# Kernel optimization log

Measured on AMD Instinct MI355X. Metric: run time of the kernel, lower is better.

The kernel has to match this reference:

```python
import jax, jax.numpy as jnp
import numpy as np

N = 50000      # nodes
E = 250000     # edges (pairs) per key
DIN = 256
DOUT = 256
OH = 16        # one_hot_length
T = 2          # params['t']


def setup_inputs() -> dict:
    key = jax.random.key(0)
    ks = jax.random.split(key, 16)
    s_in = 1.0 / np.float32(np.sqrt(DIN))
    s_tr = 1.0 / np.float32(np.sqrt(DIN + OH))
    return {
        "h": jax.random.normal(ks[0], (N, DIN), jnp.float32),
        "pairs_k0": jax.random.randint(ks[1], (T, E), 0, N),
        "pairs_k1": jax.random.randint(ks[2], (T, E), 0, N),
        "degrees_k0": jax.random.uniform(ks[3], (T, E, OH), jnp.float32),
        "degrees_k1": jax.random.uniform(ks[4], (T, E, OH), jnp.float32),
        "scatter_k0": jax.random.randint(ks[5], (E,), 0, N),
        "scatter_k1": jax.random.randint(ks[6], (E,), 0, N),
        "W_lin": jax.random.normal(ks[7], (DIN, DOUT), jnp.float32) * s_in,
        "b_lin": jax.random.normal(ks[8], (DOUT,), jnp.float32) * 0.01,
        "W_k0": jax.random.normal(ks[9], (DIN + OH, DOUT), jnp.float32) * s_tr,
        "b_k0": jax.random.normal(ks[10], (DOUT,), jnp.float32) * 0.01,
        "W_k1": jax.random.normal(ks[11], (DIN + OH, DOUT), jnp.float32) * s_tr,
        "b_k1": jax.random.normal(ks[12], (DOUT,), jnp.float32) * 0.01,
        "eps_k0": jnp.zeros((1,), jnp.float32),
        "eps_k1": jnp.zeros((1,), jnp.float32),
    }


def _key_term(h, pairs, degrees, W, b, scatter, eps):
    # combination == 'multi': product over t of sigmoid(Linear([h[pairs_i], deg_i]))
    h_temp = jnp.ones((pairs.shape[1], W.shape[1]), h.dtype)
    for i in range(T):
        h_t = jnp.concatenate([h[pairs[i]], degrees[i]], axis=1)  # [E, DIN+OH]
        h_temp = h_temp * jax.nn.sigmoid(h_t @ W + b)             # [E, DOUT]
    h_sum = jax.ops.segment_sum(h_temp, scatter, num_segments=N)  # [N, DOUT]
    return (1.0 + eps) * h_sum                                    # scalar eps (shape [1])


def reference(h, pairs_k0, pairs_k1, degrees_k0, degrees_k1,
              scatter_k0, scatter_k1, W_lin, b_lin,
              W_k0, b_k0, W_k1, b_k1, eps_k0, eps_k1):
    h3 = h @ W_lin + b_lin
    h3 = h3 + _key_term(h, pairs_k0, degrees_k0, W_k0, b_k0, scatter_k0, eps_k0)
    h3 = h3 + _key_term(h, pairs_k1, degrees_k1, W_k1, b_k1, scatter_k1, eps_k1)
    return h3
```

## Files before the change

### kernel.cpp

```cpp
#include <hip/hip_runtime.h>
#include <hip/hip_bf16.h>

#define N_NODES 50000
#define N_EDGES 250000
#define DIN_ 256
#define DOUT_ 256
#define OH_ 16
#define KF_ 288
#define NBLK_EDGE ((N_EDGES + 63) / 64)
#define SCAN_TOT (2 * N_NODES)
#define SCAN_NB ((SCAN_TOT + 255) / 256)

typedef short short8 __attribute__((ext_vector_type(8)));
typedef float f32x4 __attribute__((ext_vector_type(4)));

__device__ __forceinline__ unsigned short f2bf(float f) {
    unsigned u = __builtin_bit_cast(unsigned, f);
    return (unsigned short)((u + 0x7fffu + ((u >> 16) & 1u)) >> 16);
}

__device__ __forceinline__ uint4 pack8(float f0, float f1, float f2, float f3,
                                       float f4, float f5, float f6, float f7) {
    uint4 u;
    u.x = (unsigned)f2bf(f0) | ((unsigned)f2bf(f1) << 16);
    u.y = (unsigned)f2bf(f2) | ((unsigned)f2bf(f3) << 16);
    u.z = (unsigned)f2bf(f4) | ((unsigned)f2bf(f5) << 16);
    u.w = (unsigned)f2bf(f6) | ((unsigned)f2bf(f7) << 16);
    return u;
}

__device__ __forceinline__ float fast_rcp(float x) {
#if __has_builtin(__builtin_amdgcn_rcpf)
    return __builtin_amdgcn_rcpf(x);
#else
    return 1.0f / x;
#endif
}

__device__ __forceinline__ void gl_lds16(const void* g, void* l) {
    __builtin_amdgcn_global_load_lds(
        (const __attribute__((address_space(1))) unsigned int*)g,
        (__attribute__((address_space(3))) unsigned int*)l, 16, 0, 0);
}

__global__ void hist_kernel(const int* __restrict__ sc0, const int* __restrict__ sc1,
                            int* __restrict__ hist) {
    int e = blockIdx.x * 256 + threadIdx.x;
    if (e < N_EDGES) {
        atomicAdd(&hist[sc0[e]], 1);
        atomicAdd(&hist[N_NODES + sc1[e]], 1);
    }
}

__global__ void scan_pass1(const int* __restrict__ hist, int* __restrict__ partials) {
    __shared__ int sdata[256];
    int gid = blockIdx.x * 256 + threadIdx.x;
    sdata[threadIdx.x] = (gid < SCAN_TOT) ? hist[gid] : 0;
    __syncthreads();
    for (int d = 128; d > 0; d >>= 1) {
        if (threadIdx.x < d) sdata[threadIdx.x] += sdata[threadIdx.x + d];
        __syncthreads();
    }
    if (threadIdx.x == 0) partials[blockIdx.x] = sdata[0];
}

__global__ __launch_bounds__(512) void scan_pass2(int* __restrict__ partials) {
    __shared__ int s[512];
    int t = threadIdx.x;
    s[t] = (t < SCAN_NB) ? partials[t] : 0;
    __syncthreads();
    for (int d = 1; d < 512; d <<= 1) {
        int add = (t >= d) ? s[t - d] : 0;
        __syncthreads();
        s[t] += add;
        __syncthreads();
    }
    if (t < SCAN_NB) partials[t] = (t == 0) ? 0 : s[t - 1];
}

__global__ void scan_pass3(const int* __restrict__ hist, const int* __restrict__ partials,
                           int* __restrict__ offs) {
    __shared__ int s[256];
    int gid = blockIdx.x * 256 + threadIdx.x;
    int t = threadIdx.x;
    int v = (gid < SCAN_TOT) ? hist[gid] : 0;
    s[t] = v;
    __syncthreads();
    for (int d = 1; d < 256; d <<= 1) {
        int add = (t >= d) ? s[t - d] : 0;
        __syncthreads();
        s[t] += add;
        __syncthreads();
    }
    if (gid < SCAN_TOT) offs[gid] = partials[blockIdx.x] + s[t] - v;
}

__global__ void rank_kernel(const int* __restrict__ sc0, const int* __restrict__ sc1,
                            int* __restrict__ offs, int* __restrict__ order,
                            int* __restrict__ keys) {
    int e = blockIdx.x * 256 + threadIdx.x;
    if (e < N_EDGES) {
        int k0 = sc0[e];
        int p = atomicAdd(&offs[k0], 1);
        order[p] = e; keys[p] = k0;
        int k1 = sc1[e];
        int q = atomicAdd(&offs[N_NODES + k1], 1);
        order[q] = e; keys[q] = k1;
    }
}

__global__ void prep_weights(const float* __restrict__ W_lin,
                             const float* __restrict__ W_k0,
                             const float* __restrict__ W_k1,
                             unsigned short* __restrict__ WT_lin,
                             unsigned short* __restrict__ WT_k0,
                             unsigned short* __restrict__ WT_k1) {
    int idx = blockIdx.x * 256 + threadIdx.x;
    if (idx < DOUT_ * DIN_) {
        int n = idx >> 8, k = idx & 255;
        WT_lin[idx] = f2bf(W_lin[k * DOUT_ + n]);
    }
    if (idx < DOUT_ * KF_) {
        int n = idx / KF_, k = idx - n * KF_;
        float v0 = 0.f, v1 = 0.f;
        if (k < DIN_ + OH_) {
            v0 = W_k0[k * DOUT_ + n];
            v1 = W_k1[k * DOUT_ + n];
        }
        WT_k0[idx] = f2bf(v0);
        WT_k1[idx] = f2bf(v1);
    }
}

__global__ void conv_h(const float* __restrict__ h, unsigned short* __restrict__ hbf) {
    int idx = blockIdx.x * 256 + threadIdx.x;
    const float4* s = (const float4*)(h + (size_t)idx * 8);
    float4 a = s[0], b = s[1];
    ((uint4*)hbf)[idx] = pack8(a.x, a.y, a.z, a.w, b.x, b.y, b.z, b.w);
}

__global__ __launch_bounds__(256) void main_gemm(const unsigned short* __restrict__ hbf,
                                                 const unsigned short* __restrict__ WT,
                                                 const float* __restrict__ bias,
                                                 float* __restrict__ out) {
    __shared__ unsigned short Alds[2][64][32];
    __shared__ unsigned short Blds[2][256][32];
    __shared__ float bias_lds[256];
    int tid = threadIdx.x;
    int w = tid >> 6, ln = tid & 63, l15 = ln & 15;
    int row0 = blockIdx.x * 64;
    bias_lds[tid] = bias[tid];

    int ar = row0 + w * 16 + (ln >> 2);
    if (ar >= N_NODES) ar = N_NODES - 1;
    int qs = (ln & 3) ^ ((ln >> 3) & 3);
    const unsigned short* asrc = hbf + (size_t)ar * DIN_ + qs * 8;
    int brow = w * 64;
    int swz = ((ln >> 4) ^ ((l15 >> 1) & 3)) * 8;

    f32x4 acc[16];
#pragma unroll
    for (int j = 0; j < 16; ++j) acc[j] = (f32x4)(0.f);

    gl_lds16(asrc, &Alds[0][w * 16][0]);
#pragma unroll
    for (int i = 0; i < 4; ++i) {
        int n = brow + i * 16 + (ln >> 2);
        gl_lds16(WT + (size_t)n * DIN_ + qs * 8, &Blds[0][brow + i * 16][0]);
    }
    __syncthreads();

    int buf = 0;
    for (int kk = 0; kk < 8; ++kk) {
        if (kk < 7) {
            gl_lds16(asrc + (kk + 1) * 32, &Alds[buf ^ 1][w * 16][0]);
#pragma unroll
            for (int i = 0; i < 4; ++i) {
                int n = brow + i * 16 + (ln >> 2);
                gl_lds16(WT + (size_t)n * DIN_ + (kk + 1) * 32 + qs * 8,
                         &Blds[buf ^ 1][brow + i * 16][0]);
            }
        }
        short8 af = *(const short8*)&Alds[buf][w * 16 + l15][swz];
#pragma unroll
        for (int j = 0; j < 16; ++j) {
            short8 bf = *(const short8*)&Blds[buf][j * 16 + l15][swz];
            acc[j] = __builtin_amdgcn_mfma_f32_16x16x32_bf16(af, bf, acc[j], 0, 0, 0);
        }
        __syncthreads();
        buf ^= 1;
    }

    int rbase = row0 + w * 16 + ((ln >> 4) << 2);
#pragma unroll
    for (int j = 0; j < 16; ++j) {
        int n = j * 16 + l15;
        float bv = bias_lds[n];
#pragma unroll
        for (int i = 0; i < 4; ++i) {
            int rr = rbase + i;
            if (rr < N_NODES) out[(size_t)rr * DOUT_ + n] = acc[j][i] + bv;
        }
    }
}

__global__ __launch_bounds__(256) void edge_gemm(const unsigned short* __restrict__ hbf,
                                                 const int* __restrict__ pairs0,
                                                 const int* __restrict__ pairs1,
                                                 const float* __restrict__ deg0,
                                                 const float* __restrict__ deg1,
                                                 const int* __restrict__ order_all,
                                                 const int* __restrict__ keys_all,
                                                 const unsigned short* __restrict__ WT0,
                                                 const unsigned short* __restrict__ WT1,
                                                 const float* __restrict__ bias0,
                                                 const float* __restrict__ bias1,
                                                 const float* __restrict__ eps0,
                                                 const float* __restrict__ eps1,
                                                 float* __restrict__ out) {
    __shared__ unsigned short Alds[2][2][64][32];
    __shared__ unsigned short Blds[2][256][32];
    __shared__ float bias_lds[256];
    __shared__ int tgt[64];
    int kb = (blockIdx.x >= NBLK_EDGE) ? 1 : 0;
    int bx = blockIdx.x - kb * NBLK_EDGE;
    const int* pairs = kb ? pairs1 : pairs0;
    const float* degrees = kb ? deg1 : deg0;
    const int* order_k = order_all + kb * N_EDGES;
    const int* keys_k  = keys_all + kb * N_EDGES;
    const unsigned short* WT = kb ? WT1 : WT0;
    const float* bias = kb ? bias1 : bias0;
    const float* eps  = kb ? eps1 : eps0;

    int tid = threadIdx.x;
    int w = tid >> 6, ln = tid & 63, l15 = ln & 15;
    int e0 = bx * 64;
    bias_lds[tid] = bias[tid];
    if (tid < 64) {
        int s = e0 + tid;
        tgt[tid] = (s < N_EDGES) ? keys_k[s] : -1;
    }

    int sA = e0 + w * 16 + (ln >> 2);
    if (sA >= N_EDGES) sA = N_EDGES - 1;
    int eA = order_k[sA];
    int p0 = pairs[eA];
    int p1 = pairs[N_EDGES + eA];
    int qs = (ln & 3) ^ ((ln >> 3) & 3);
    const unsigned short* a0src = hbf + (size_t)p0 * DIN_ + qs * 8;
    const unsigned short* a1src = hbf + (size_t)p1 * DIN_ + qs * 8;
    int brow = w * 64;
    int swz = ((ln >> 4) ^ ((l15 >> 1) & 3)) * 8;

    int r8 = tid >> 2, q8 = tid & 3;
    int m8 = (q8 ^ ((r8 >> 1) & 3)) * 8;
    int s8 = e0 + r8;
    if (s8 >= N_EDGES) s8 = N_EDGES - 1;
    int e8 = order_k[s8];

    f32x4 acc0[16], acc1[16];
#pragma unroll
    for (int j = 0; j < 16; ++j) { acc0[j] = (f32x4)(0.f); acc1[j] = (f32x4)(0.f); }

    gl_lds16(a0src, &Alds[0][0][w * 16][0]);
    gl_lds16(a1src, &Alds[0][1][w * 16][0]);
#pragma unroll
    for (int i = 0; i < 4; ++i) {
        int n = brow + i * 16 + (ln >> 2);
        gl_lds16(WT + (size_t)n * KF_ + qs * 8, &Blds[0][brow + i * 16][0]);
    }
    __syncthreads();

    int buf = 0;
    for (int kk = 0; kk < 9; ++kk) {
        if (kk < 8) {
#pragma unroll
            for (int i = 0; i < 4; ++i) {
                int n = brow + i * 16 + (ln >> 2);
                gl_lds16(WT + (size_t)n * KF_ + (kk + 1) * 32 + qs * 8,
                         &Blds[buf ^ 1][brow + i * 16][0]);
            }
            if (kk < 7) {
                gl_lds16(a0src + (kk + 1) * 32, &Alds[buf ^ 1][0][w * 16][0]);
                gl_lds16(a1src + (kk + 1) * 32, &Alds[buf ^ 1][1][w * 16][0]);
            } else {
#pragma unroll
                for (int t = 0; t < 2; ++t) {
                    uint4 v = make_uint4(0u, 0u, 0u, 0u);
                    if (q8 < 2) {
                        const float4* s4 = (const float4*)(degrees +
                            ((size_t)t * N_EDGES + e8) * OH_ + q8 * 8);
                        float4 a = s4[0], b = s4[1];
                        v = pack8(a.x, a.y, a.z, a.w, b.x, b.y, b.z, b.w);
                    }
                    *(uint4*)&Alds[buf ^ 1][t][r8][m8] = v;
                }
            }
        }
        short8 a0f = *(const short8*)&Alds[buf][0][w * 16 + l15][swz];
        short8 a1f = *(const short8*)&Alds[buf][1][w * 16 + l15][swz];
#pragma unroll
        for (int j = 0; j < 16; ++j) {
            short8 bf = *(const short8*)&Blds[buf][j * 16 + l15][swz];
            acc0[j] = __builtin_amdgcn_mfma_f32_16x16x32_bf16(a0f, bf, acc0[j], 0, 0, 0);
            acc1[j] = __builtin_amdgcn_mfma_f32_16x16x32_bf16(a1f, bf, acc1[j], 0, 0, 0);
        }
        __syncthreads();
        buf ^= 1;
    }

    float* red = (float*)&Blds[0][0][0];
    float epv = 1.0f + eps[0];
    int rloc = w * 16 + ((ln >> 4) << 2);
    int c = tid & 63, Rb = (tid >> 6) * 16;

#pragma unroll
    for (int jc = 0; jc < 4; ++jc) {
#pragma unroll
        for (int jj = 0; jj < 4; ++jj) {
            float bv = bias_lds[(jc * 4 + jj) * 16 + l15];
#pragma unroll
            for (int i = 0; i < 4; ++i) {
                int row = rloc + i;
                float v = 0.f;
                if (e0 + row < N_EDGES) {
                    float a = acc0[jc * 4 + jj][i] + bv;
                    float b = acc1[jc * 4 + jj][i] + bv;
                    float ea = __expf(-a), eb = __expf(-b);
                    v = epv * fast_rcp((1.f + ea) * (1.f + eb));
                }
                red[row * 68 + jj * 16 + l15] = v;
            }
        }
        __syncthreads();
        int n = jc * 64 + c;
        int runkey = tgt[Rb];
        float runsum = red[Rb * 68 + c];
        for (int r = Rb + 1; r < Rb + 16; ++r) {
            int k = tgt[r];
            float val = red[r * 68 + c];
            if (k != runkey) {
                if (runkey >= 0) atomicAdd(&out[(size_t)runkey * DOUT_ + n], runsum);
                runkey = k;
                runsum = val;
            } else {
                runsum += val;
            }
        }
        if (runkey >= 0) atomicAdd(&out[(size_t)runkey * DOUT_ + n], runsum);
        __syncthreads();
    }
}

extern "C" void kernel_launch(void* const* d_in, const int* in_sizes, int n_in,
                              void* d_out, int out_size, void* d_ws, size_t ws_size,
                              hipStream_t stream) {
    const float* h        = (const float*)d_in[0];
    const int*   pairs_k0 = (const int*)d_in[1];
    const int*   pairs_k1 = (const int*)d_in[2];
    const float* deg_k0   = (const float*)d_in[3];
    const float* deg_k1   = (const float*)d_in[4];
    const int*   sc_k0    = (const int*)d_in[5];
    const int*   sc_k1    = (const int*)d_in[6];
    const float* W_lin    = (const float*)d_in[7];
    const float* b_lin    = (const float*)d_in[8];
    const float* W_k0     = (const float*)d_in[9];
    const float* b_k0     = (const float*)d_in[10];
    const float* W_k1     = (const float*)d_in[11];
    const float* b_k1     = (const float*)d_in[12];
    const float* eps_k0   = (const float*)d_in[13];
    const float* eps_k1   = (const float*)d_in[14];
    float* out = (float*)d_out;

    size_t ush_elems = (size_t)DOUT_ * DIN_ + 2 * (size_t)DOUT_ * KF_ + (size_t)N_NODES * DIN_;
    size_t int_elems = 2 * (size_t)N_NODES * 2 + 2 * (size_t)N_EDGES * 2 + 512;
    size_t need = ush_elems * sizeof(unsigned short) + int_elems * sizeof(int);
    if (ws_size < need) return;

    unsigned short* WT_lin = (unsigned short*)d_ws;
    unsigned short* WT_k0  = WT_lin + DOUT_ * DIN_;
    unsigned short* WT_k1  = WT_k0 + DOUT_ * KF_;
    unsigned short* h_bf   = WT_k1 + DOUT_ * KF_;
    int* hist     = (int*)(h_bf + (size_t)N_NODES * DIN_);
    int* offs     = hist + 2 * N_NODES;
    int* order    = offs + 2 * N_NODES;
    int* keys     = order + 2 * N_EDGES;
    int* partials = keys + 2 * N_EDGES;

    hipMemsetAsync(hist, 0, 2 * N_NODES * sizeof(int), stream);
    hist_kernel<<<(N_EDGES + 255) / 256, 256, 0, stream>>>(sc_k0, sc_k1, hist);
    scan_pass1<<<SCAN_NB, 256, 0, stream>>>(hist, partials);
    scan_pass2<<<1, 512, 0, stream>>>(partials);
    scan_pass3<<<SCAN_NB, 256, 0, stream>>>(hist, partials, offs);
    rank_kernel<<<(N_EDGES + 255) / 256, 256, 0, stream>>>(sc_k0, sc_k1, offs, order, keys);

    prep_weights<<<(DOUT_ * KF_ + 255) / 256, 256, 0, stream>>>(W_lin, W_k0, W_k1,
                                                                WT_lin, WT_k0, WT_k1);
    conv_h<<<(N_NODES * DIN_ / 8) / 256, 256, 0, stream>>>(h, h_bf);
    main_gemm<<<(N_NODES + 63) / 64, 256, 0, stream>>>(h_bf, WT_lin, b_lin, out);
    edge_gemm<<<2 * NBLK_EDGE, 256, 0, stream>>>(h_bf, pairs_k0, pairs_k1, deg_k0, deg_k1,
                                                 order, keys, WT_k0, WT_k1, b_k0, b_k1,
                                                 eps_k0, eps_k1, out);
}
```

Baseline: 426.2 us.

## Precompute per-node h@W projections and gather them in the edge kernel

Because h[pairs]@W[:256] equals (h@W[:256])[pairs], a new per-node GEMM computes G = h@W + b for each key once over the 50000 nodes and stores it in bf16. The edge kernel then only does the small 16-wide degree GEMM per edge and gathers G rows for both pair endpoints before the sigmoid product and segmented atomic reduction. This removes the 250000x256x256 per-edge GEMM in exchange for a node GEMM, extra workspace, bf16 rounding of G, and scattered 2-byte gathers from G.

Result: no change. 427.1 us (+0.2%).

```diff
diff --git a/kernel.cpp b/kernel.cpp
--- a/kernel.cpp
+++ b/kernel.cpp
@@ -8,6 +8,7 @@
 #define OH_ 16
 #define KF_ 288
 #define NBLK_EDGE ((N_EDGES + 63) / 64)
+#define NBLK_G ((N_NODES + 63) / 64)
 #define SCAN_TOT (2 * N_NODES)
 #define SCAN_NB ((SCAN_TOT + 255) / 256)
 
@@ -17,6 +18,10 @@
 __device__ __forceinline__ unsigned short f2bf(float f) {
     unsigned u = __builtin_bit_cast(unsigned, f);
     return (unsigned short)((u + 0x7fffu + ((u >> 16) & 1u)) >> 16);
+}
+
+__device__ __forceinline__ float bf2f(unsigned short v) {
+    return __builtin_bit_cast(float, (unsigned)v << 16);
 }
 
 __device__ __forceinline__ uint4 pack8(float f0, float f1, float f2, float f3,
@@ -204,151 +209,189 @@
     }
 }
 
-__global__ __launch_bounds__(256) void edge_gemm(const unsigned short* __restrict__ hbf,
-                                                 const int* __restrict__ pairs0,
-                                                 const int* __restrict__ pairs1,
-                                                 const float* __restrict__ deg0,
-                                                 const float* __restrict__ deg1,
-                                                 const int* __restrict__ order_all,
-                                                 const int* __restrict__ keys_all,
-                                                 const unsigned short* __restrict__ WT0,
-                                                 const unsigned short* __restrict__ WT1,
-                                                 const float* __restrict__ bias0,
-                                                 const float* __restrict__ bias1,
-                                                 const float* __restrict__ eps0,
-                                                 const float* __restrict__ eps1,
-                                                 float* __restrict__ out) {
-    __shared__ unsigned short Alds[2][2][64][32];
+__global__ __launch_bounds__(256) void g_gemm(const unsigned short* __restrict__ hbf,
+                                              const unsigned short* __restrict__ WT0,
+                                              const unsigned short* __restrict__ WT1,
+                                              const float* __restrict__ b0,
+                                              const float* __restrict__ b1,
+                                              unsigned short* __restrict__ G0,
+                                              unsigned short* __restrict__ G1) {
+    __shared__ unsigned short Alds[2][64][32];
     __shared__ unsigned short Blds[2][256][32];
     __shared__ float bias_lds[256];
-    __shared__ int tgt[64];
+    int kb = (blockIdx.x >= NBLK_G) ? 1 : 0;
+    int bx = blockIdx.x - kb * NBLK_G;
+    const unsigned short* WT = kb ? WT1 : WT0;
+    const float* bias = kb ? b1 : b0;
+    unsigned short* G = kb ? G1 : G0;
+
+    int tid = threadIdx.x;
+    int w = tid >> 6, ln = tid & 63, l15 = ln & 15;
+    int row0 = bx * 64;
+    bias_lds[tid] = bias[tid];
+
+    int ar = row0 + w * 16 + (ln >> 2);
+    if (ar >= N_NODES) ar = N_NODES - 1;
+    int qs = (ln & 3) ^ ((ln >> 3) & 3);
+    const unsigned short* asrc = hbf + (size_t)ar * DIN_ + qs * 8;
+    int brow = w * 64;
+    int swz = ((ln >> 4) ^ ((l15 >> 1) & 3)) * 8;
+
+    f32x4 acc[16];
+#pragma unroll
+    for (int j = 0; j < 16; ++j) acc[j] = (f32x4)(0.f);
+
+    gl_lds16(asrc, &Alds[0][w * 16][0]);
+#pragma unroll
+    for (int i = 0; i < 4; ++i) {
+        int n = brow + i * 16 + (ln >> 2);
+        gl_lds16(WT + (size_t)n * KF_ + qs * 8, &Blds[0][brow + i * 16][0]);
+    }
+    __syncthreads();
+
+    int buf = 0;
+    for (int kk = 0; kk < 8; ++kk) {
+        if (kk < 7) {
+            gl_lds16(asrc + (kk + 1) * 32, &Alds[buf ^ 1][w * 16][0]);
+#pragma unroll
+            for (int i = 0; i < 4; ++i) {
+                int n = brow + i * 16 + (ln >> 2);
+                gl_lds16(WT + (size_t)n * KF_ + (kk + 1) * 32 + qs * 8,
+                         &Blds[buf ^ 1][brow + i * 16][0]);
+            }
+        }
+        short8 af = *(const short8*)&Alds[buf][w * 16 + l15][swz];
+#pragma unroll
+        for (int j = 0; j < 16; ++j) {
+            short8 bf = *(const short8*)&Blds[buf][j * 16 + l15][swz];
+            acc[j] = __builtin_amdgcn_mfma_f32_16x16x32_bf16(af, bf, acc[j], 0, 0, 0);
+        }
+        __syncthreads();
+        buf ^= 1;
+    }
+
+    int rbase = row0 + w * 16 + ((ln >> 4) << 2);
+#pragma unroll
+    for (int j = 0; j < 16; ++j) {
+        int n = j * 16 + l15;
+        float bv = bias_lds[n];
+#pragma unroll
+        for (int i = 0; i < 4; ++i) {
+            int rr = rbase + i;
+            if (rr < N_NODES) G[(size_t)rr * DOUT_ + n] = f2bf(acc[j][i] + bv);
+        }
+    }
+}
+
+__global__ __launch_bounds__(256) void edge_fused(const unsigned short* __restrict__ Gk0,
+                                                  const unsigned short* __restrict__ Gk1,
+                                                  const int* __restrict__ pairs0,
+                                                  const int* __restrict__ pairs1,
+                                                  const float* __restrict__ deg0,
+                                                  const float* __restrict__ deg1,
+                                                  const int* __restrict__ order_all,
+                                                  const int* __restrict__ keys_all,
+                                                  const unsigned short* __restrict__ WT0,
+                                                  const unsigned short* __restrict__ WT1,
+                                                  const float* __restrict__ eps0,
+                                                  const float* __restrict__ eps1,
+                                                  float* __restrict__ out) {
+    __shared__ float red0[64][68];
+    __shared__ float red1[64][68];
+    __shared__ int tgt[64], pl0[64], pl1[64], el[64];
     int kb = (blockIdx.x >= NBLK_EDGE) ? 1 : 0;
     int bx = blockIdx.x - kb * NBLK_EDGE;
+    const unsigned short* G = kb ? Gk1 : Gk0;
     const int* pairs = kb ? pairs1 : pairs0;
     const float* degrees = kb ? deg1 : deg0;
     const int* order_k = order_all + kb * N_EDGES;
     const int* keys_k  = keys_all + kb * N_EDGES;
     const unsigned short* WT = kb ? WT1 : WT0;
-    const float* bias = kb ? bias1 : bias0;
-    const float* eps  = kb ? eps1 : eps0;
+    float epv = 1.0f + (kb ? eps1[0] : eps0[0]);
 
     int tid = threadIdx.x;
-    int w = tid >> 6, ln = tid & 63, l15 = ln & 15;
+    int w = tid >> 6, ln = tid & 63, l15 = ln & 15, ks = ln >> 4;
     int e0 = bx * 64;
-    bias_lds[tid] = bias[tid];
     if (tid < 64) {
         int s = e0 + tid;
+        int sc = (s < N_EDGES) ? s : N_EDGES - 1;
+        int e = order_k[sc];
+        el[tid]  = e;
         tgt[tid] = (s < N_EDGES) ? keys_k[s] : -1;
-    }
-
-    int sA = e0 + w * 16 + (ln >> 2);
-    if (sA >= N_EDGES) sA = N_EDGES - 1;
-    int eA = order_k[sA];
-    int p0 = pairs[eA];
-    int p1 = pairs[N_EDGES + eA];
-    int qs = (ln & 3) ^ ((ln >> 3) & 3);
-    const unsigned short* a0src = hbf + (size_t)p0 * DIN_ + qs * 8;
-    const unsigned short* a1src = hbf + (size_t)p1 * DIN_ + qs * 8;
-    int brow = w * 64;
-    int swz = ((ln >> 4) ^ ((l15 >> 1) & 3)) * 8;
-
-    int r8 = tid >> 2, q8 = tid & 3;
-    int m8 = (q8 ^ ((r8 >> 1) & 3)) * 8;
-    int s8 = e0 + r8;
-    if (s8 >= N_EDGES) s8 = N_EDGES - 1;
-    int e8 = order_k[s8];
-
-    f32x4 acc0[16], acc1[16];
-#pragma unroll
-    for (int j = 0; j < 16; ++j) { acc0[j] = (f32x4)(0.f); acc1[j] = (f32x4)(0.f); }
-
-    gl_lds16(a0src, &Alds[0][0][w * 16][0]);
-    gl_lds16(a1src, &Alds[0][1][w * 16][0]);
-#pragma unroll
-    for (int i = 0; i < 4; ++i) {
-        int n = brow + i * 16 + (ln >> 2);
-        gl_lds16(WT + (size_t)n * KF_ + qs * 8, &Blds[0][brow + i * 16][0]);
-    }
-    __syncthreads();
-
-    int buf = 0;
-    for (int kk = 0; kk < 9; ++kk) {
-        if (kk < 8) {
-#pragma unroll
-            for (int i = 0; i < 4; ++i) {
-                int n = brow + i * 16 + (ln >> 2);
-                gl_lds16(WT + (size_t)n * KF_ + (kk + 1) * 32 + qs * 8,
-                         &Blds[buf ^ 1][brow + i * 16][0]);
-            }
-            if (kk < 7) {
-                gl_lds16(a0src + (kk + 1) * 32, &Alds[buf ^ 1][0][w * 16][0]);
-                gl_lds16(a1src + (kk + 1) * 32, &Alds[buf ^ 1][1][w * 16][0]);
-            } else {
-#pragma unroll
-                for (int t = 0; t < 2; ++t) {
-                    uint4 v = make_uint4(0u, 0u, 0u, 0u);
-                    if (q8 < 2) {
-                        const float4* s4 = (const float4*)(degrees +
-                            ((size_t)t * N_EDGES + e8) * OH_ + q8 * 8);
-                        float4 a = s4[0], b = s4[1];
-                        v = pack8(a.x, a.y, a.z, a.w, b.x, b.y, b.z, b.w);
-                    }
-                    *(uint4*)&Alds[buf ^ 1][t][r8][m8] = v;
+        pl0[tid] = pairs[e];
+        pl1[tid] = pairs[N_EDGES + e];
+    }
+    __syncthreads();
+
+    int eA = el[w * 16 + l15];
+    short8 a0f = (short8)0, a1f = (short8)0;
+    if (ks < 2) {
+        const float4* s0 = (const float4*)(degrees + ((size_t)0 * N_EDGES + eA) * OH_ + ks * 8);
+        const float4* s1 = (const float4*)(degrees + ((size_t)1 * N_EDGES + eA) * OH_ + ks * 8);
+        float4 xa = s0[0], xb = s0[1];
+        float4 ya = s1[0], yb = s1[1];
+        a0f = __builtin_bit_cast(short8, pack8(xa.x, xa.y, xa.z, xa.w, xb.x, xb.y, xb.z, xb.w));
+        a1f = __builtin_bit_cast(short8, pack8(ya.x, ya.y, ya.z, ya.w, yb.x, yb.y, yb.z, yb.w));
+    }
+
+    int c = ln;
+    int Rb = w * 16;
+
+#pragma unroll
+    for (int half = 0; half < 2; ++half) {
+        f32x4 acc0[8], acc1[8];
+#pragma unroll
+        for (int j = 0; j < 8; ++j) { acc0[j] = (f32x4)(0.f); acc1[j] = (f32x4)(0.f); }
+#pragma unroll
+        for (int j = 0; j < 8; ++j) {
+            int n = half * 128 + j * 16 + l15;
+            short8 bf = (short8)0;
+            if (ks < 2) bf = *(const short8*)(WT + (size_t)n * KF_ + 256 + ks * 8);
+            acc0[j] = __builtin_amdgcn_mfma_f32_16x16x32_bf16(a0f, bf, acc0[j], 0, 0, 0);
+            acc1[j] = __builtin_amdgcn_mfma_f32_16x16x32_bf16(a1f, bf, acc1[j], 0, 0, 0);
+        }
+#pragma unroll
+        for (int jc = 0; jc < 2; ++jc) {
+#pragma unroll
+            for (int jj = 0; jj < 4; ++jj) {
+#pragma unroll
+                for (int i = 0; i < 4; ++i) {
+                    int row = w * 16 + ks * 4 + i;
+                    red0[row][jj * 16 + l15] = acc0[jc * 4 + jj][i];
+                    red1[row][jj * 16 + l15] = acc1[jc * 4 + jj][i];
                 }
             }
-        }
-        short8 a0f = *(const short8*)&Alds[buf][0][w * 16 + l15][swz];
-        short8 a1f = *(const short8*)&Alds[buf][1][w * 16 + l15][swz];
-#pragma unroll
-        for (int j = 0; j < 16; ++j) {
-            short8 bf = *(const short8*)&Blds[buf][j * 16 + l15][swz];
-            acc0[j] = __builtin_amdgcn_mfma_f32_16x16x32_bf16(a0f, bf, acc0[j], 0, 0, 0);
-            acc1[j] = __builtin_amdgcn_mfma_f32_16x16x32_bf16(a1f, bf, acc1[j], 0, 0, 0);
-        }
-        __syncthreads();
-        buf ^= 1;
-    }
-
-    float* red = (float*)&Blds[0][0][0];
-    float epv = 1.0f + eps[0];
-    int rloc = w * 16 + ((ln >> 4) << 2);
-    int c = tid & 63, Rb = (tid >> 6) * 16;
-
-#pragma unroll
-    for (int jc = 0; jc < 4; ++jc) {
-#pragma unroll
-        for (int jj = 0; jj < 4; ++jj) {
-            float bv = bias_lds[(jc * 4 + jj) * 16 + l15];
-#pragma unroll
-            for (int i = 0; i < 4; ++i) {
-                int row = rloc + i;
-                float v = 0.f;
-                if (e0 + row < N_EDGES) {
-                    float a = acc0[jc * 4 + jj][i] + bv;
-                    float b = acc1[jc * 4 + jj][i] + bv;
-                    float ea = __expf(-a), eb = __expf(-b);
-                    v = epv * fast_rcp((1.f + ea) * (1.f + eb));
+            __syncthreads();
+            int n = half * 128 + jc * 64 + c;
+            int runkey = tgt[Rb];
+            float runsum;
+            {
+                float g0 = bf2f(G[(size_t)pl0[Rb] * DOUT_ + n]);
+                float g1 = bf2f(G[(size_t)pl1[Rb] * DOUT_ + n]);
+                float ea = __expf(-(g0 + red0[Rb][c]));
+                float eb = __expf(-(g1 + red1[Rb][c]));
+                runsum = epv * fast_rcp((1.f + ea) * (1.f + eb));
+            }
+#pragma unroll
+            for (int rr = 1; rr < 16; ++rr) {
+                int r = Rb + rr;
+                float g0 = bf2f(G[(size_t)pl0[r] * DOUT_ + n]);
+                float g1 = bf2f(G[(size_t)pl1[r] * DOUT_ + n]);
+                float ea = __expf(-(g0 + red0[r][c]));
+                float eb = __expf(-(g1 + red1[r][c]));
+                float val = epv * fast_rcp((1.f + ea) * (1.f + eb));
+                int k = tgt[r];
+                if (k != runkey) {
+                    if (runkey >= 0) atomicAdd(&out[(size_t)runkey * DOUT_ + n], runsum);
+                    runkey = k;
+                    runsum = val;
+                } else {
+                    runsum += val;
                 }
-                red[row * 68 + jj * 16 + l15] = v;
             }
-        }
-        __syncthreads();
-        int n = jc * 64 + c;
-        int runkey = tgt[Rb];
-        float runsum = red[Rb * 68 + c];
-        for (int r = Rb + 1; r < Rb + 16; ++r) {
-            int k = tgt[r];
-            float val = red[r * 68 + c];
-            if (k != runkey) {
-                if (runkey >= 0) atomicAdd(&out[(size_t)runkey * DOUT_ + n], runsum);
-                runkey = k;
-                runsum = val;
-            } else {
-                runsum += val;
-            }
-        }
-        if (runkey >= 0) atomicAdd(&out[(size_t)runkey * DOUT_ + n], runsum);
-        __syncthreads();
+            if (runkey >= 0) atomicAdd(&out[(size_t)runkey * DOUT_ + n], runsum);
+            __syncthreads();
+        }
     }
 }
 
@@ -372,7 +415,8 @@
     const float* eps_k1   = (const float*)d_in[14];
     float* out = (float*)d_out;
 
-    size_t ush_elems = (size_t)DOUT_ * DIN_ + 2 * (size_t)DOUT_ * KF_ + (size_t)N_NODES * DIN_;
+    size_t ush_elems = (size_t)DOUT_ * DIN_ + 2 * (size_t)DOUT_ * KF_
+                     + 3 * (size_t)N_NODES * DIN_;
     size_t int_elems = 2 * (size_t)N_NODES * 2 + 2 * (size_t)N_EDGES * 2 + 512;
     size_t need = ush_elems * sizeof(unsigned short) + int_elems * sizeof(int);
     if (ws_size < need) return;
@@ -381,7 +425,9 @@
     unsigned short* WT_k0  = WT_lin + DOUT_ * DIN_;
     unsigned short* WT_k1  = WT_k0 + DOUT_ * KF_;
     unsigned short* h_bf   = WT_k1 + DOUT_ * KF_;
-    int* hist     = (int*)(h_bf + (size_t)N_NODES * DIN_);
+    unsigned short* G0     = h_bf + (size_t)N_NODES * DIN_;
+    unsigned short* G1     = G0 + (size_t)N_NODES * DIN_;
+    int* hist     = (int*)(G1 + (size_t)N_NODES * DIN_);
     int* offs     = hist + 2 * N_NODES;
     int* order    = offs + 2 * N_NODES;
     int* keys     = order + 2 * N_EDGES;
@@ -397,8 +443,9 @@
     prep_weights<<<(DOUT_ * KF_ + 255) / 256, 256, 0, stream>>>(W_lin, W_k0, W_k1,
                                                                 WT_lin, WT_k0, WT_k1);
     conv_h<<<(N_NODES * DIN_ / 8) / 256, 256, 0, stream>>>(h, h_bf);
-    main_gemm<<<(N_NODES + 63) / 64, 256, 0, stream>>>(h_bf, WT_lin, b_lin, out);
-    edge_gemm<<<2 * NBLK_EDGE, 256, 0, stream>>>(h_bf, pairs_k0, pairs_k1, deg_k0, deg_k1,
-                                                 order, keys, WT_k0, WT_k1, b_k0, b_k1,
-                                                 eps_k0, eps_k1, out);
-}
+    main_gemm<<<NBLK_G, 256, 0, stream>>>(h_bf, WT_lin, b_lin, out);
+    g_gemm<<<2 * NBLK_G, 256, 0, stream>>>(h_bf, WT_k0, WT_k1, b_k0, b_k1, G0, G1);
+    edge_fused<<<2 * NBLK_EDGE, 256, 0, stream>>>(G0, G1, pairs_k0, pairs_k1,
+                                                  deg_k0, deg_k1, order, keys,
+                                                  WT_k0, WT_k1, eps_k0, eps_k1, out);
+}
```
